# Kernel tuning notes

Measured on AMD Instinct MI355X. Metric: run time of the kernel, lower is better.

Reference implementation:

```python
import jax, jax.numpy as jnp
import numpy as np

E = 8
D_IN = 1024
D_HID = 4096
D_OUT = 1024
N_TOK = 32768  # total tokens; equal split of 4096 per expert


def setup_inputs() -> dict:
    key = jax.random.key(0)
    k_in, k_w1, k_w2 = jax.random.split(key, 3)
    inputs = jax.random.normal(k_in, (N_TOK, D_IN), dtype=jnp.float32)
    expert_size = jnp.full((E,), N_TOK // E, dtype=jnp.int64)
    # reset_parameters: normal(0, 1/sqrt(fan_in)) per expert
    w1 = jax.random.normal(k_w1, (E, D_IN, D_HID), dtype=jnp.float32) / np.sqrt(D_IN)
    b1 = jnp.zeros((E, D_HID), dtype=jnp.float32)
    w2 = jax.random.normal(k_w2, (E, D_HID, D_OUT), dtype=jnp.float32) / np.sqrt(D_HID)
    b2 = jnp.zeros((E, D_OUT), dtype=jnp.float32)
    return {"inputs": inputs, "expert_size": expert_size,
            "w1": w1, "b1": b1, "w2": w2, "b2": b2}


def reference(inputs, expert_size, w1, b1, w2, b2):
    # Grouped GEMM over contiguous per-expert splits. expert_size is equal
    # per expert (N_TOK // E), so the variable-split loop in the torch code
    # collapses to a batched einsum with identical math.
    e = w1.shape[0]
    n, d = inputs.shape
    cap = n // e  # tokens per expert (equal splits)
    x = inputs.reshape(e, cap, d)                       # [E, cap, D_IN]
    h = jnp.einsum('ecd,edh->ech', x, w1) + b1[:, None, :]
    h = jax.nn.gelu(h, approximate=False)               # F.gelu default = erf gelu
    y = jnp.einsum('ech,eho->eco', h, w2) + b2[:, None, :]
    return y.reshape(n, -1)                             # [N_TOK, D_OUT]
```

## Files before the change

kernel.cpp:

```cpp
#include <hip/hip_runtime.h>
#include <hip/hip_bf16.h>
#include <type_traits>

#define NE 8
#define DIN 1024
#define DHID 4096
#define DOUTD 1024
#define NTOK 32768
#define CAP (NTOK / NE)

typedef unsigned short u16;
typedef __attribute__((ext_vector_type(8))) short bf16x8;
typedef __attribute__((ext_vector_type(4))) float f32x4;

__device__ __forceinline__ u16 f2bf(float x) {
  unsigned u = __builtin_bit_cast(unsigned, x);
  u += 0x7fffu + ((u >> 16) & 1u);
  return (u16)(u >> 16);
}

__device__ __forceinline__ float gelu_erf(float x) {
  return 0.5f * x * (1.0f + erff(x * 0.70710678118654752f));
}

__device__ __forceinline__ void async_ld16(const void* g, void* l) {
  __builtin_amdgcn_global_load_lds(
      (const __attribute__((address_space(1))) unsigned int*)g,
      (__attribute__((address_space(3))) unsigned int*)l, 16, 0, 0);
}

__global__ __launch_bounds__(256) void convert_bf16_kernel(const float* __restrict__ in,
                                                           u16* __restrict__ out) {
  size_t i = ((size_t)blockIdx.x * 256 + threadIdx.x) * 8;
  float4 a = *(const float4*)(in + i);
  float4 b = *(const float4*)(in + i + 4);
  uint4 o;
  o.x = (unsigned)f2bf(a.x) | ((unsigned)f2bf(a.y) << 16);
  o.y = (unsigned)f2bf(a.z) | ((unsigned)f2bf(a.w) << 16);
  o.z = (unsigned)f2bf(b.x) | ((unsigned)f2bf(b.y) << 16);
  o.w = (unsigned)f2bf(b.z) | ((unsigned)f2bf(b.w) << 16);
  *(uint4*)(out + i) = o;
}

__global__ __launch_bounds__(256) void transpose_bf16_kernel(const float* __restrict__ in,
                                                             u16* __restrict__ out,
                                                             int K, int N) {
  __shared__ __align__(16) u16 tile[64 * 72];
  const int e = blockIdx.z;
  const int n0 = blockIdx.x * 64;
  const int k0 = blockIdx.y * 64;
  const float* inp = in + (size_t)e * K * N;
  u16* outp = out + (size_t)e * N * K;
  const int t = threadIdx.x;
  const int kr = t >> 4;
  const int nc = (t & 15) * 4;
#pragma unroll
  for (int rr = 0; rr < 4; ++rr) {
    int kl = rr * 16 + kr;
    float4 v = *(const float4*)(inp + (size_t)(k0 + kl) * N + n0 + nc);
    tile[(nc + 0) * 72 + kl] = f2bf(v.x);
    tile[(nc + 1) * 72 + kl] = f2bf(v.y);
    tile[(nc + 2) * 72 + kl] = f2bf(v.z);
    tile[(nc + 3) * 72 + kl] = f2bf(v.w);
  }
  __syncthreads();
  const int nr = t >> 3;
  const int kc = (t & 7) * 8;
#pragma unroll
  for (int it = 0; it < 2; ++it) {
    int nl = it * 32 + nr;
    bf16x8 w = *(const bf16x8*)(tile + nl * 72 + kc);
    *(bf16x8*)(outp + (size_t)(n0 + nl) * K + k0 + kc) = w;
  }
}

template <int K, int N, bool GELU_OUT>
__global__ __launch_bounds__(512, 2) void moe_gemm256_kernel(
    const u16* __restrict__ A, const u16* __restrict__ Bt,
    const float* __restrict__ bias, void* __restrict__ Out) {
  extern __shared__ __align__(16) char smem[];
  constexpr int TX = N / 256;
  constexpr int NT = K / 32;

  const int bid = blockIdx.x;
  const int e = bid & 7;
  const int idx = bid >> 3;
  const int ty = idx / TX;
  const int tx = idx % TX;
  const int m0 = ty * 256;
  const int n0 = tx * 256;

  const u16* Ae = A + (size_t)e * CAP * K;
  const u16* Be = Bt + (size_t)e * N * K;

  const int t = threadIdx.x;
  const int l = t & 63;
  const int w = t >> 6;
  const int wr = w >> 2;
  const int wc = w & 3;
  const int g = l >> 4;
  const int rl = l & 15;

  const int ul = (l & 7) ^ (l >> 3);
  const int skk = (ul & 3) * 8;
  const int srhi = (ul >> 2) << 7;
  size_t sa[2], sb[2];
  int chunkbase[2];
#pragma unroll
  for (int it = 0; it < 2; ++it) {
    int chunk = it * 8 + w;
    int rowp = chunk * 8 + (l >> 3);
    sa[it] = (size_t)(m0 + rowp + srhi) * K + skk;
    sb[it] = (size_t)(n0 + rowp + srhi) * K + skk;
    chunkbase[it] = chunk * 1024;
  }

  int aoff[8], boff[4];
#pragma unroll
  for (int j = 0; j < 8; ++j) {
    int rp = j * 16 + rl;
    aoff[j] = rp * 128 + (((wr * 4 + g) ^ (rl & 7)) << 4);
  }
#pragma unroll
  for (int i = 0; i < 4; ++i) {
    int rp = (wc & 1) * 64 + i * 16 + rl;
    boff[i] = 16384 + rp * 128 + ((((wc >> 1) * 4 + g) ^ (rl & 7)) << 4);
  }

  f32x4 acc[8][4] = {};

  auto stage = [&](int tt) {
    char* dst = smem + (size_t)(tt & 3) * 32768;
    const size_t kb = (size_t)tt * 32;
#pragma unroll
    for (int it = 0; it < 2; ++it)
      async_ld16(Ae + sa[it] + kb, dst + chunkbase[it]);
#pragma unroll
    for (int it = 0; it < 2; ++it)
      async_ld16(Be + sb[it] + kb, dst + 16384 + chunkbase[it]);
  };

  stage(0);
  stage(1);
  stage(2);
  asm volatile("s_waitcnt vmcnt(8)\n\ts_barrier" ::: "memory");

  auto kiter = [&](int tt, auto STG, auto WN) {
    if constexpr (decltype(STG)::value) stage(tt + 3);
    const char* src = smem + (size_t)(tt & 3) * 32768;
    bf16x8 afr[8], bfr[4];
#pragma unroll
    for (int i = 0; i < 4; ++i) bfr[i] = *(const bf16x8*)(src + boff[i]);
#pragma unroll
    for (int j = 0; j < 8; ++j) afr[j] = *(const bf16x8*)(src + aoff[j]);
    __builtin_amdgcn_s_setprio(1);
#pragma unroll
    for (int j = 0; j < 8; ++j)
#pragma unroll
      for (int i = 0; i < 4; ++i)
        acc[j][i] = __builtin_amdgcn_mfma_f32_16x16x32_bf16(bfr[i], afr[j], acc[j][i], 0, 0, 0);
    __builtin_amdgcn_s_setprio(0);
    constexpr int WNv = decltype(WN)::value;
    if constexpr (WNv >= 0) {
      asm volatile("s_waitcnt vmcnt(%0)\n\ts_barrier" :: "n"(WNv) : "memory");
    }
  };

  for (int tt = 0; tt < NT - 3; ++tt)
    kiter(tt, std::true_type{}, std::integral_constant<int, 8>{});
  kiter(NT - 3, std::false_type{}, std::integral_constant<int, 4>{});
  kiter(NT - 2, std::false_type{}, std::integral_constant<int, 0>{});
  kiter(NT - 1, std::false_type{}, std::integral_constant<int, -1>{});

  const float* be = bias + (size_t)e * N;
  const int mb = m0 + wr * 128 + rl;
  const int nb = n0 + wc * 64 + g * 4;
  if constexpr (GELU_OUT) {
    u16* Oe = (u16*)Out + (size_t)e * (size_t)CAP * N;
#pragma unroll
    for (int j = 0; j < 8; ++j) {
      int m = mb + j * 16;
#pragma unroll
      for (int i = 0; i < 4; ++i) {
        int n = nb + i * 16;
        float4 bv = *(const float4*)(be + n);
        ushort4 o;
        o.x = f2bf(gelu_erf(acc[j][i][0] + bv.x));
        o.y = f2bf(gelu_erf(acc[j][i][1] + bv.y));
        o.z = f2bf(gelu_erf(acc[j][i][2] + bv.z));
        o.w = f2bf(gelu_erf(acc[j][i][3] + bv.w));
        *(ushort4*)(Oe + (size_t)m * N + n) = o;
      }
    }
  } else {
    float* Oe = (float*)Out + (size_t)e * (size_t)CAP * N;
#pragma unroll
    for (int j = 0; j < 8; ++j) {
      int m = mb + j * 16;
#pragma unroll
      for (int i = 0; i < 4; ++i) {
        int n = nb + i * 16;
        float4 bv = *(const float4*)(be + n);
        float4 o;
        o.x = acc[j][i][0] + bv.x;
        o.y = acc[j][i][1] + bv.y;
        o.z = acc[j][i][2] + bv.z;
        o.w = acc[j][i][3] + bv.w;
        *(float4*)(Oe + (size_t)m * N + n) = o;
      }
    }
  }
}

extern "C" void kernel_launch(void* const* d_in, const int* in_sizes, int n_in,
                              void* d_out, int out_size, void* d_ws, size_t ws_size,
                              hipStream_t stream) {
  const float* x  = (const float*)d_in[0];
  const float* w1 = (const float*)d_in[2];
  const float* b1 = (const float*)d_in[3];
  const float* w2 = (const float*)d_in[4];
  const float* b2 = (const float*)d_in[5];
  float* out = (float*)d_out;

  char* wsp = (char*)d_ws;
  u16* x_bf = (u16*)(wsp);
  u16* w1t  = (u16*)(wsp + (size_t)67108864);
  u16* w2t  = (u16*)(wsp + (size_t)134217728);
  u16* h    = (u16*)(wsp + (size_t)201326592);

  hipFuncSetAttribute(reinterpret_cast<const void*>(moe_gemm256_kernel<DIN, DHID, true>),
                      hipFuncAttributeMaxDynamicSharedMemorySize, 131072);
  hipFuncSetAttribute(reinterpret_cast<const void*>(moe_gemm256_kernel<DHID, DOUTD, false>),
                      hipFuncAttributeMaxDynamicSharedMemorySize, 131072);

  convert_bf16_kernel<<<(NTOK * DIN) / (256 * 8), 256, 0, stream>>>(x, x_bf);
  transpose_bf16_kernel<<<dim3(DHID / 64, DIN / 64, NE), 256, 0, stream>>>(w1, w1t, DIN, DHID);
  transpose_bf16_kernel<<<dim3(DOUTD / 64, DHID / 64, NE), 256, 0, stream>>>(w2, w2t, DHID, DOUTD);

  moe_gemm256_kernel<DIN, DHID, true>
      <<<dim3(NE * (CAP / 256) * (DHID / 256)), 512, 131072, stream>>>(x_bf, w1t, b1, h);
  moe_gemm256_kernel<DHID, DOUTD, false>
      <<<dim3(NE * (CAP / 256) * (DOUTD / 256)), 512, 131072, stream>>>(h, w2t, b2, out);
}
```

Baseline: 781.9 us.

## Restructure GEMM main loop into three-stage ping-pong pipeline with split A fragments

Replaces the four-buffer, three-deep prefetch pipeline with a three-buffer, two-deep pipeline. Each k-step is split into two halves: A and B async loads are interleaved with the LDS fragment reads and MFMA blocks, and barriers sit between the halves. Loading A fragments in two groups of four lowers register pressure, and LDS use drops from 128 KiB to 96 KiB. The shallower prefetch and the extra barriers risk exposing global-load latency and adding sync overhead.

```diff
diff --git a/kernel.cpp b/kernel.cpp
--- a/kernel.cpp
+++ b/kernel.cpp
@@ -1,6 +1,5 @@
 #include <hip/hip_runtime.h>
 #include <hip/hip_bf16.h>
-#include <type_traits>
 
 #define NE 8
 #define DIN 1024
@@ -78,99 +77,111 @@
 __global__ __launch_bounds__(512, 2) void moe_gemm256_kernel(
     const u16* __restrict__ A, const u16* __restrict__ Bt,
     const float* __restrict__ bias, void* __restrict__ Out) {
-  extern __shared__ __align__(16) char smem[];
+  extern __shared__ __align__(16) char sm[];
   constexpr int TX = N / 256;
   constexpr int NT = K / 32;
 
   const int bid = blockIdx.x;
   const int e = bid & 7;
   const int idx = bid >> 3;
-  const int ty = idx / TX;
-  const int tx = idx % TX;
-  const int m0 = ty * 256;
-  const int n0 = tx * 256;
+  const int m0 = (idx / TX) * 256;
+  const int n0 = (idx % TX) * 256;
 
   const u16* Ae = A + (size_t)e * CAP * K;
   const u16* Be = Bt + (size_t)e * N * K;
 
-  const int t = threadIdx.x;
-  const int l = t & 63;
-  const int w = t >> 6;
+  const int tid = threadIdx.x;
+  const int l = tid & 63;
+  const int w = tid >> 6;
   const int wr = w >> 2;
   const int wc = w & 3;
   const int g = l >> 4;
   const int rl = l & 15;
 
-  const int ul = (l & 7) ^ (l >> 3);
-  const int skk = (ul & 3) * 8;
-  const int srhi = (ul >> 2) << 7;
-  size_t sa[2], sb[2];
-  int chunkbase[2];
-#pragma unroll
-  for (int it = 0; it < 2; ++it) {
-    int chunk = it * 8 + w;
-    int rowp = chunk * 8 + (l >> 3);
-    sa[it] = (size_t)(m0 + rowp + srhi) * K + skk;
-    sb[it] = (size_t)(n0 + rowp + srhi) * K + skk;
-    chunkbase[it] = chunk * 1024;
-  }
-
-  int aoff[8], boff[4];
-#pragma unroll
-  for (int j = 0; j < 8; ++j) {
-    int rp = j * 16 + rl;
-    aoff[j] = rp * 128 + (((wr * 4 + g) ^ (rl & 7)) << 4);
+  int aoff0[4], aoff1[4], boff[4];
+#pragma unroll
+  for (int q = 0; q < 4; ++q) {
+    aoff0[q] = (q * 16 + rl) * 128 + ((((wr << 2) + g) ^ (rl & 7)) << 4);
+    aoff1[q] = aoff0[q] + 64 * 128;
   }
 #pragma unroll
   for (int i = 0; i < 4; ++i) {
-    int rp = (wc & 1) * 64 + i * 16 + rl;
-    boff[i] = 16384 + rp * 128 + ((((wc >> 1) * 4 + g) ^ (rl & 7)) << 4);
-  }
+    int row = wc * 64 + i * 16 + rl;
+    boff[i] = 16384 + (row & 127) * 128 + (((((row >> 7) << 2) + g) ^ (rl & 7)) << 4);
+  }
+
+  auto mkoff = [&](int sidx, int base0) -> size_t {
+    int lrow = sidx >> 3, ucol = sidx & 7;
+    int lu = ucol ^ (lrow & 7);
+    int r = lrow + ((lu & 4) << 5);
+    return (size_t)(base0 + r) * K + (lu & 3) * 8;
+  };
+  const size_t sA0 = mkoff(tid, m0), sA1 = mkoff(512 + tid, m0);
+  const size_t sB0 = mkoff(tid, n0), sB1 = mkoff(512 + tid, n0);
+  const int dA0 = tid * 16, dA1 = 8192 + tid * 16;
+  const int dB0 = 16384 + tid * 16, dB1 = 24576 + tid * 16;
 
   f32x4 acc[8][4] = {};
 
-  auto stage = [&](int tt) {
-    char* dst = smem + (size_t)(tt & 3) * 32768;
-    const size_t kb = (size_t)tt * 32;
-#pragma unroll
-    for (int it = 0; it < 2; ++it)
-      async_ld16(Ae + sa[it] + kb, dst + chunkbase[it]);
-#pragma unroll
-    for (int it = 0; it < 2; ++it)
-      async_ld16(Be + sb[it] + kb, dst + 16384 + chunkbase[it]);
-  };
-
-  stage(0);
-  stage(1);
-  stage(2);
-  asm volatile("s_waitcnt vmcnt(8)\n\ts_barrier" ::: "memory");
-
-  auto kiter = [&](int tt, auto STG, auto WN) {
-    if constexpr (decltype(STG)::value) stage(tt + 3);
-    const char* src = smem + (size_t)(tt & 3) * 32768;
-    bf16x8 afr[8], bfr[4];
-#pragma unroll
-    for (int i = 0; i < 4; ++i) bfr[i] = *(const bf16x8*)(src + boff[i]);
-#pragma unroll
-    for (int j = 0; j < 8; ++j) afr[j] = *(const bf16x8*)(src + aoff[j]);
+  async_ld16(Ae + sA0, sm + dA0);
+  async_ld16(Ae + sA1, sm + dA1);
+  async_ld16(Be + sB0, sm + dB0);
+  async_ld16(Be + sB1, sm + dB1);
+  async_ld16(Ae + sA0 + 32, sm + 32768 + dA0);
+  async_ld16(Ae + sA1 + 32, sm + 32768 + dA1);
+  async_ld16(Be + sB0 + 32, sm + 32768 + dB0);
+  async_ld16(Be + sB1 + 32, sm + 32768 + dB1);
+  asm volatile("s_waitcnt vmcnt(4)\n\ts_barrier" ::: "memory");
+
+  int b0 = 0, b1 = 32768, b2 = 65536;
+
+#pragma unroll 1
+  for (int tt = 0; tt < NT; ++tt) {
+    const bool st = (tt + 2 < NT);
+    const size_t kb2 = (size_t)(tt + 2) * 32;
+    bf16x8 afr[4], bfr[4];
+    if (st) {
+      async_ld16(Ae + sA0 + kb2, sm + b2 + dA0);
+      async_ld16(Ae + sA1 + kb2, sm + b2 + dA1);
+    }
+#pragma unroll
+    for (int i = 0; i < 4; ++i) bfr[i] = *(const bf16x8*)(sm + b0 + boff[i]);
+#pragma unroll
+    for (int q = 0; q < 4; ++q) afr[q] = *(const bf16x8*)(sm + b0 + aoff0[q]);
+    __builtin_amdgcn_s_barrier();
+    asm volatile("s_waitcnt lgkmcnt(0)" ::: "memory");
+    __builtin_amdgcn_sched_barrier(0);
     __builtin_amdgcn_s_setprio(1);
 #pragma unroll
-    for (int j = 0; j < 8; ++j)
+    for (int q = 0; q < 4; ++q)
 #pragma unroll
       for (int i = 0; i < 4; ++i)
-        acc[j][i] = __builtin_amdgcn_mfma_f32_16x16x32_bf16(bfr[i], afr[j], acc[j][i], 0, 0, 0);
+        acc[q][i] = __builtin_amdgcn_mfma_f32_16x16x32_bf16(bfr[i], afr[q], acc[q][i], 0, 0, 0);
     __builtin_amdgcn_s_setprio(0);
-    constexpr int WNv = decltype(WN)::value;
-    if constexpr (WNv >= 0) {
-      asm volatile("s_waitcnt vmcnt(%0)\n\ts_barrier" :: "n"(WNv) : "memory");
-    }
-  };
-
-  for (int tt = 0; tt < NT - 3; ++tt)
-    kiter(tt, std::true_type{}, std::integral_constant<int, 8>{});
-  kiter(NT - 3, std::false_type{}, std::integral_constant<int, 4>{});
-  kiter(NT - 2, std::false_type{}, std::integral_constant<int, 0>{});
-  kiter(NT - 1, std::false_type{}, std::integral_constant<int, -1>{});
+    __builtin_amdgcn_s_barrier();
+    if (st) {
+      async_ld16(Be + sB0 + kb2, sm + b2 + dB0);
+      async_ld16(Be + sB1 + kb2, sm + b2 + dB1);
+    }
+#pragma unroll
+    for (int q = 0; q < 4; ++q) afr[q] = *(const bf16x8*)(sm + b0 + aoff1[q]);
+    __builtin_amdgcn_s_barrier();
+    asm volatile("s_waitcnt lgkmcnt(0)" ::: "memory");
+    __builtin_amdgcn_sched_barrier(0);
+    __builtin_amdgcn_s_setprio(1);
+#pragma unroll
+    for (int q = 0; q < 4; ++q)
+#pragma unroll
+      for (int i = 0; i < 4; ++i)
+        acc[4 + q][i] = __builtin_amdgcn_mfma_f32_16x16x32_bf16(bfr[i], afr[q], acc[4 + q][i], 0, 0, 0);
+    __builtin_amdgcn_s_setprio(0);
+    if (tt < NT - 2) {
+      asm volatile("s_waitcnt vmcnt(3)\n\ts_barrier" ::: "memory");
+    } else if (tt == NT - 2) {
+      asm volatile("s_waitcnt vmcnt(0)\n\ts_barrier" ::: "memory");
+    }
+    int tmp = b0; b0 = b1; b1 = b2; b2 = tmp;
+  }
 
   const float* be = bias + (size_t)e * N;
   const int mb = m0 + wr * 128 + rl;
@@ -229,16 +240,16 @@
   u16* h    = (u16*)(wsp + (size_t)201326592);
 
   hipFuncSetAttribute(reinterpret_cast<const void*>(moe_gemm256_kernel<DIN, DHID, true>),
-                      hipFuncAttributeMaxDynamicSharedMemorySize, 131072);
+                      hipFuncAttributeMaxDynamicSharedMemorySize, 98304);
   hipFuncSetAttribute(reinterpret_cast<const void*>(moe_gemm256_kernel<DHID, DOUTD, false>),
-                      hipFuncAttributeMaxDynamicSharedMemorySize, 131072);
+                      hipFuncAttributeMaxDynamicSharedMemorySize, 98304);
 
   convert_bf16_kernel<<<(NTOK * DIN) / (256 * 8), 256, 0, stream>>>(x, x_bf);
   transpose_bf16_kernel<<<dim3(DHID / 64, DIN / 64, NE), 256, 0, stream>>>(w1, w1t, DIN, DHID);
   transpose_bf16_kernel<<<dim3(DOUTD / 64, DHID / 64, NE), 256, 0, stream>>>(w2, w2t, DHID, DOUTD);
 
   moe_gemm256_kernel<DIN, DHID, true>
-      <<<dim3(NE * (CAP / 256) * (DHID / 256)), 512, 131072, stream>>>(x_bf, w1t, b1, h);
+      <<<dim3(NE * (CAP / 256) * (DHID / 256)), 512, 98304, stream>>>(x_bf, w1t, b1, h);
   moe_gemm256_kernel<DHID, DOUTD, false>
-      <<<dim3(NE * (CAP / 256) * (DOUTD / 256)), 512, 131072, stream>>>(h, w2t, b2, out);
-}
+      <<<dim3(NE * (CAP / 256) * (DOUTD / 256)), 512, 98304, stream>>>(h, w2t, b2, out);
+}
```

After: 797.8 us. +2.0%, slower.
